# Performance work log

Hardware: AMD Instinct MI355X
Metric: run time of the kernel (lower is better)

The kernel has to match this reference:

```python
import jax, jax.numpy as jnp
import numpy as np

WS = 7          # window size
HN = 6          # heads
C = 192         # emb dim
SHIFT = WS >> 1
L = WS * WS


def _rel_index(ws):
    c = np.stack(np.meshgrid(np.arange(ws), np.arange(ws), indexing='ij'), -1).reshape(-1, 2)
    d = c[:, None, :] - c[None, :, :] + (ws - 1)
    return jnp.asarray(d[..., 0] * (2 * ws - 1) + d[..., 1])  # (L, L) int


def _shift_mask(ws, shift):
    # after intra-window roll by -shift, positions >= ws-shift are wrapped pixels
    r = (np.arange(ws) >= ws - shift).astype(np.int32)
    rid = (2 * r[:, None] + r[None, :]).reshape(-1)  # (L,) region id
    m = np.where(rid[:, None] != rid[None, :], -100.0, 0.0).astype(np.float32)
    return jnp.asarray(m)  # (L, L)


def _ln(x, g, b, eps=1e-5):
    m = jnp.mean(x, -1, keepdims=True)
    v = jnp.mean(jnp.square(x - m), -1, keepdims=True)
    return (x - m) * jax.lax.rsqrt(v + eps) * g + b


def _wmsa(x, qkv_w, qkv_b, proj_w, proj_b, bias_table, rel_idx, mask):
    N, wn, Lx, Cx = x.shape
    dh = Cx // HN
    qkv = x @ qkv_w + qkv_b                      # (N, wn, L, 3C)
    q, k, v = jnp.split(qkv, 3, axis=-1)
    q = q.reshape(N, wn, Lx, HN, dh) * (dh ** -0.5)
    k = k.reshape(N, wn, Lx, HN, dh)
    v = v.reshape(N, wn, Lx, HN, dh)
    a = jnp.einsum('nwqhd,nwkhd->nwhqk', q, k)   # (N, wn, H, L, L)
    a = a + jnp.transpose(bias_table[rel_idx], (2, 0, 1))  # (H, L, L) bias
    if mask is not None:
        a = a + mask                             # (L, L) broadcast
    a = jax.nn.softmax(a, axis=-1)
    o = jnp.einsum('nwhqk,nwkhd->nwqhd', a, v).reshape(N, wn, Lx, Cx)
    return o @ proj_w + proj_b


def _layer(X, g1, b1, g2, b2, qkv_w, qkv_b, proj_w, proj_b, bias_table, rel_idx,
           w1, bb1, w2, bb2, mask):
    tmp = _ln(X, g1, b1)
    tmp = _wmsa(tmp, qkv_w, qkv_b, proj_w, proj_b, bias_table, rel_idx, mask)
    X = _ln(X + tmp, g2, b2)  # drop_path is identity in eval
    h = jax.nn.gelu(X @ w1 + bb1, approximate=False)
    return X + (h @ w2 + bb2)


def setup_inputs() -> dict:
    key = jax.random.key(0)
    ks = jax.random.split(key, 16)
    N, wn = 8, 1024
    s = 0.02
    d = {}
    d['X'] = jax.random.normal(ks[0], (N, wn, L, C), jnp.float32)
    d['ln1_g'] = jnp.ones((C,), jnp.float32)
    d['ln1_b'] = jnp.zeros((C,), jnp.float32)
    d['ln2_g'] = jnp.ones((C,), jnp.float32)
    d['ln2_b'] = jnp.zeros((C,), jnp.float32)
    d['win_qkv_w'] = jax.random.normal(ks[1], (C, 3 * C), jnp.float32) * s
    d['win_qkv_b'] = jnp.zeros((3 * C,), jnp.float32)
    d['win_proj_w'] = jax.random.normal(ks[2], (C, C), jnp.float32) * s
    d['win_proj_b'] = jnp.zeros((C,), jnp.float32)
    d['win_bias'] = jax.random.normal(ks[3], ((2 * WS - 1) ** 2, HN), jnp.float32) * s
    d['swin_qkv_w'] = jax.random.normal(ks[4], (C, 3 * C), jnp.float32) * s
    d['swin_qkv_b'] = jnp.zeros((3 * C,), jnp.float32)
    d['swin_proj_w'] = jax.random.normal(ks[5], (C, C), jnp.float32) * s
    d['swin_proj_b'] = jnp.zeros((C,), jnp.float32)
    d['swin_bias'] = jax.random.normal(ks[6], ((2 * WS - 1) ** 2, HN), jnp.float32) * s
    d['mlp_w1'] = jax.random.normal(ks[7], (C, 4 * C), jnp.float32) * s
    d['mlp_b1'] = jnp.zeros((4 * C,), jnp.float32)
    d['mlp_w2'] = jax.random.normal(ks[8], (4 * C, C), jnp.float32) * s
    d['mlp_b2'] = jnp.zeros((C,), jnp.float32)
    return d


def reference(X, ln1_g, ln1_b, ln2_g, ln2_b,
              win_qkv_w, win_qkv_b, win_proj_w, win_proj_b, win_bias,
              swin_qkv_w, swin_qkv_b, swin_proj_w, swin_proj_b, swin_bias,
              mlp_w1, mlp_b1, mlp_w2, mlp_b2):
    rel_idx = _rel_index(WS)
    mask = _shift_mask(WS, SHIFT)
    N, wn = X.shape[0], X.shape[1]
    # block 1: plain window MSA
    X = _layer(X, ln1_g, ln1_b, ln2_g, ln2_b, win_qkv_w, win_qkv_b, win_proj_w,
               win_proj_b, win_bias, rel_idx, mlp_w1, mlp_b1, mlp_w2, mlp_b2, None)
    # intra-window cyclic shift (torch dims (-2,-3) = W,H axes)
    X = X.reshape(N, wn, WS, WS, C)
    X = jnp.roll(X, (-SHIFT, -SHIFT), axis=(3, 2))
    X = X.reshape(N, wn, L, C)
    # block 2: shifted window MSA with mask
    X = _layer(X, ln1_g, ln1_b, ln2_g, ln2_b, swin_qkv_w, swin_qkv_b, swin_proj_w,
               swin_proj_b, swin_bias, rel_idx, mlp_w1, mlp_b1, mlp_w2, mlp_b2, mask)
    # reverse roll — repo uses dims (-1,-2) = (C, W) axes; replicated faithfully
    X = X.reshape(N, wn, WS, WS, C)
    X = jnp.roll(X, (SHIFT, SHIFT), axis=(4, 3))
    return X.reshape(N, wn, L, C)
```

## Files before the change

### kernel.cpp

```cpp
#include <hip/hip_runtime.h>
#include <hip/hip_bf16.h>
#include <math.h>

#define NTOK 401408
#define NWIN 8192
#define NCHUNK 4
#define TOK_PER_CHUNK (NTOK / NCHUNK)
#define WIN_PER_CHUNK (NWIN / NCHUNK)

typedef __attribute__((ext_vector_type(8))) short bf16x8_t;
typedef __attribute__((ext_vector_type(4))) float f32x4_t;

__device__ __forceinline__ float bf2f(unsigned int u) {
    return __uint_as_float(u << 16);
}
__device__ __forceinline__ unsigned short f2bf(float f) {
    unsigned int x = __float_as_uint(f);
    x += 0x7fffu + ((x >> 16) & 1u);
    return (unsigned short)(x >> 16);
}
__device__ __forceinline__ unsigned int pack2bf(float a, float b) {
    return (unsigned int)f2bf(a) | ((unsigned int)f2bf(b) << 16);
}

__global__ void wt_all_kernel(const float* __restrict__ s0, const float* __restrict__ s1,
                              const float* __restrict__ s2, const float* __restrict__ s3,
                              const float* __restrict__ s4, const float* __restrict__ s5,
                              unsigned short* __restrict__ d0, unsigned short* __restrict__ d1,
                              unsigned short* __restrict__ d2, unsigned short* __restrict__ d3,
                              unsigned short* __restrict__ d4, unsigned short* __restrict__ d5) {
    int seg = blockIdx.y;
    const float* W; unsigned short* WT; int K, N;
    switch (seg) {
        case 0:  W = s0; WT = d0; K = 192; N = 576; break;
        case 1:  W = s1; WT = d1; K = 192; N = 576; break;
        case 2:  W = s2; WT = d2; K = 192; N = 192; break;
        case 3:  W = s3; WT = d3; K = 192; N = 192; break;
        case 4:  W = s4; WT = d4; K = 192; N = 768; break;
        default: W = s5; WT = d5; K = 768; N = 192; break;
    }
    int i = blockIdx.x * 256 + threadIdx.x;
    if (i >= N * K) return;
    int n = i / K, k = i - n * K;
    WT[i] = f2bf(W[(size_t)k * N + n]);
}

__global__ void bias_kernel(const float* __restrict__ bt0, const float* __restrict__ bt1,
                            float* __restrict__ bm) {
    int idx = blockIdx.x * 256 + threadIdx.x;
    int variant = blockIdx.y;
    const float* bt = variant ? bt1 : bt0;
    int r = idx & 3, lane = (idx >> 2) & 63, ni = (idx >> 8) & 3, mi = (idx >> 10) & 3, h = idx >> 12;
    int g = lane >> 4;
    int q = ni * 16 + (lane & 15);
    int k = mi * 16 + g * 4 + r;
    float v = 0.f;
    if (q < 49 && k < 49) {
        int qh = q / 7, qw = q - qh * 7, kh = k / 7, kw = k - kh * 7;
        v = bt[((qh - kh + 6) * 13 + (qw - kw + 6)) * 6 + h];
        if (variant) {
            int rq = 2 * (qh >= 4) + (qw >= 4), rk = 2 * (kh >= 4) + (kw >= 4);
            if (rq != rk) v -= 100.f;
        }
    }
    bm[(size_t)variant * 24576 + idx] = v;
}

template<int IN_BF16, int ROLL>
__global__ __launch_bounds__(256) void ln_kernel(const void* __restrict__ in,
                                                 unsigned short* __restrict__ out,
                                                 const float* __restrict__ g,
                                                 const float* __restrict__ b) {
    int tok  = blockIdx.x * 4 + (threadIdx.x >> 6);
    int lane = threadIdx.x & 63;
    int src = tok;
    if (ROLL) {
        int win = tok / 49, p2 = tok - win * 49;
        int h = p2 / 7, w = p2 - h * 7;
        int h2 = h + 3; if (h2 >= 7) h2 -= 7;
        int w2 = w + 3; if (w2 >= 7) w2 -= 7;
        src = win * 49 + h2 * 7 + w2;
    }
    float x0, x1, x2;
    if (IN_BF16) {
        const unsigned short* p = (const unsigned short*)in + (size_t)src * 192;
        x0 = bf2f(p[lane]); x1 = bf2f(p[lane + 64]); x2 = bf2f(p[lane + 128]);
    } else {
        const float* p = (const float*)in + (size_t)src * 192;
        x0 = p[lane]; x1 = p[lane + 64]; x2 = p[lane + 128];
    }
    float s  = x0 + x1 + x2;
    float sq = x0 * x0 + x1 * x1 + x2 * x2;
    for (int o = 32; o; o >>= 1) { s += __shfl_xor(s, o); sq += __shfl_xor(sq, o); }
    float m   = s * (1.f / 192.f);
    float var = sq * (1.f / 192.f) - m * m;
    float r   = rsqrtf(var + 1e-5f);
    unsigned short* q = out + (size_t)tok * 192;
    q[lane]       = f2bf((x0 - m) * r * g[lane]       + b[lane]);
    q[lane + 64]  = f2bf((x1 - m) * r * g[lane + 64]  + b[lane + 64]);
    q[lane + 128] = f2bf((x2 - m) * r * g[lane + 128] + b[lane + 128]);
}

#define EP_QKV        0
#define EP_PROJ1      1
#define EP_PROJ2      2
#define EP_MLP1       3
#define EP_MLP2_TRUNK 4
#define EP_MLP2_OUT   5

template<int NDIM, int KDIM, int NY, int EP>
__global__ __launch_bounds__(256) void gemm_kernel(const unsigned short* __restrict__ A,
                                                   const unsigned short* __restrict__ WT,
                                                   const float* __restrict__ bias,
                                                   const void* __restrict__ res,
                                                   void* __restrict__ out,
                                                   int row0) {
    __shared__ __align__(16) unsigned short As[128][40];
    __shared__ __align__(16) unsigned short Bs[96][40];
    int tid = threadIdx.x;
    int nwg = gridDim.x;
    int id = blockIdx.x;
    int id2 = (id & 7) * (nwg >> 3) + (id >> 3);
    int by = id2 % NY, bx = id2 / NY;
    int rowBase = bx * 128;
    int colBase = by * 96;

    int cr = tid >> 2, cp = (tid & 3) * 8;
    const unsigned short* Ab = A  + (size_t)rowBase * KDIM + cp;
    const unsigned short* Bb = WT + (size_t)colBase * KDIM + cp;

    uint4 a0, a1, b0, b1;
    const int NT = KDIM / 32;

    #define LOADK(k0)                                                          \
        do {                                                                   \
            a0 = *(const uint4*)(Ab + (size_t)cr * KDIM + (k0));               \
            a1 = *(const uint4*)(Ab + (size_t)(cr + 64) * KDIM + (k0));        \
            b0 = *(const uint4*)(Bb + (size_t)cr * KDIM + (k0));               \
            if (tid < 128) b1 = *(const uint4*)(Bb + (size_t)(cr + 64) * KDIM + (k0)); \
        } while (0)
    #define WRITEK()                                                           \
        do {                                                                   \
            *(uint4*)&As[cr][cp] = a0;                                         \
            *(uint4*)&As[cr + 64][cp] = a1;                                    \
            *(uint4*)&Bs[cr][cp] = b0;                                         \
            if (tid < 128) *(uint4*)&Bs[cr + 64][cp] = b1;                     \
        } while (0)

    LOADK(0);

    int wave = tid >> 6, lane = tid & 63;
    int wm = wave >> 1, wn = wave & 1;
    int kq = lane >> 4, lr = lane & 15;

    f32x4_t acc[4][3] = {};
    for (int kt = 0; kt < NT; ++kt) {
        __syncthreads();
        WRITEK();
        if (kt + 1 < NT) LOADK((kt + 1) * 32);
        __syncthreads();
        bf16x8_t afr[4], bfr[3];
        #pragma unroll
        for (int mi = 0; mi < 4; ++mi)
            afr[mi] = *(const bf16x8_t*)&As[wm * 64 + mi * 16 + lr][kq * 8];
        #pragma unroll
        for (int ni = 0; ni < 3; ++ni)
            bfr[ni] = *(const bf16x8_t*)&Bs[wn * 48 + ni * 16 + lr][kq * 8];
        #pragma unroll
        for (int mi = 0; mi < 4; ++mi)
            #pragma unroll
            for (int ni = 0; ni < 3; ++ni)
                acc[mi][ni] = __builtin_amdgcn_mfma_f32_16x16x32_bf16(
                    afr[mi], bfr[ni], acc[mi][ni], 0, 0, 0);
    }
    #undef LOADK
    #undef WRITEK

    const float* resf = (const float*)res;
    const unsigned short* resb = (const unsigned short*)res;
    #pragma unroll
    for (int mi = 0; mi < 4; ++mi) {
        #pragma unroll
        for (int ni = 0; ni < 3; ++ni) {
            int col = colBase + wn * 48 + ni * 16 + lr;
            float bcol = bias[col];
            #pragma unroll
            for (int r = 0; r < 4; ++r) {
                int rloc = rowBase + wm * 64 + mi * 16 + kq * 4 + r;
                float v = acc[mi][ni][r] + bcol;
                if (EP == EP_QKV) {
                    if (colBase < 192) v *= 0.17677669529663687f;
                    ((unsigned short*)out)[(size_t)rloc * NDIM + col] = f2bf(v);
                } else if (EP == EP_PROJ1) {
                    v += resf[(size_t)rloc * 192 + col];
                    ((unsigned short*)out)[(size_t)rloc * 192 + col] = f2bf(v);
                } else if (EP == EP_PROJ2) {
                    int win = rloc / 49, p2 = rloc - win * 49;
                    int h = p2 / 7, w = p2 - h * 7;
                    int h2 = h + 3; if (h2 >= 7) h2 -= 7;
                    int w2 = w + 3; if (w2 >= 7) w2 -= 7;
                    v += bf2f((unsigned int)resb[((size_t)win * 49 + h2 * 7 + w2) * 192 + col]);
                    ((unsigned short*)out)[(size_t)rloc * 192 + col] = f2bf(v);
                } else if (EP == EP_MLP1) {
                    float u2 = v * (1.59576912f + 0.0713548162f * v * v);
                    float e  = __expf(u2);
                    float gl = v - v * __builtin_amdgcn_rcpf(e + 1.f);
                    ((unsigned short*)out)[(size_t)rloc * NDIM + col] = f2bf(gl);
                } else if (EP == EP_MLP2_TRUNK) {
                    v += bf2f((unsigned int)resb[(size_t)rloc * 192 + col]);
                    int grow = row0 + rloc;
                    ((unsigned short*)out)[(size_t)grow * 192 + col] = f2bf(v);
                } else {
                    v += bf2f((unsigned int)resb[(size_t)rloc * 192 + col]);
                    int grow = row0 + rloc;
                    int win = grow / 49, p2 = grow - win * 49;
                    int h = p2 / 7, w = p2 - h * 7;
                    int w2 = w + 3; if (w2 >= 7) w2 -= 7;
                    int c2 = col + 3; if (c2 >= 192) c2 -= 192;
                    ((float*)out)[((size_t)win * 49 + h * 7 + w2) * 192 + c2] = v;
                }
            }
        }
    }
}

__global__ __launch_bounds__(64) void attn_kernel(const unsigned short* __restrict__ qkv,
                                                  const float* __restrict__ bm,
                                                  unsigned short* __restrict__ outp,
                                                  int win0) {
    __shared__ unsigned short P[64][72];
    __shared__ unsigned short VT[32][72];
    int head = blockIdx.x, wloc = blockIdx.y;
    int lane = threadIdx.x;
    int g = lane >> 4, lr = lane & 15;
    const unsigned short* base = qkv + (size_t)wloc * 49 * 576;

    for (int i = lane; i < 256; i += 64) {
        int tok = i >> 2, seg = i & 3;
        uint4 u = make_uint4(0u, 0u, 0u, 0u);
        if (tok < 49)
            u = *(const uint4*)(base + (size_t)tok * 576 + 384 + head * 32 + seg * 8);
        const unsigned short* us = (const unsigned short*)&u;
        #pragma unroll
        for (int j = 0; j < 8; ++j) VT[seg * 8 + j][tok] = us[j];
    }

    bf16x8_t kf[4], qf[4];
    #pragma unroll
    for (int mi = 0; mi < 4; ++mi) {
        int tok = mi * 16 + lr; if (tok > 48) tok = 48;
        kf[mi] = *(const bf16x8_t*)(base + (size_t)tok * 576 + 192 + head * 32 + g * 8);
    }
    #pragma unroll
    for (int ni = 0; ni < 4; ++ni) {
        int tok = ni * 16 + lr; if (tok > 48) tok = 48;
        qf[ni] = *(const bf16x8_t*)(base + (size_t)tok * 576 + head * 32 + g * 8);
    }

    const float* bmh = bm + (size_t)head * 4096;
    f32x4_t acc[4][4];
    #pragma unroll
    for (int mi = 0; mi < 4; ++mi)
        #pragma unroll
        for (int ni = 0; ni < 4; ++ni)
            acc[mi][ni] = *(const f32x4_t*)(bmh + ((mi * 4 + ni) * 64 + lane) * 4);
    #pragma unroll
    for (int mi = 0; mi < 4; ++mi)
        #pragma unroll
        for (int ni = 0; ni < 4; ++ni)
            acc[mi][ni] = __builtin_amdgcn_mfma_f32_16x16x32_bf16(kf[mi], qf[ni], acc[mi][ni], 0, 0, 0);

    float inv[4];
    #pragma unroll
    for (int ni = 0; ni < 4; ++ni) {
        float mx = -1e30f;
        #pragma unroll
        for (int mi = 0; mi < 3; ++mi)
            #pragma unroll
            for (int r = 0; r < 4; ++r) mx = fmaxf(mx, acc[mi][ni][r]);
        mx = fmaxf(mx, (g == 0) ? acc[3][ni][0] : -1e30f);
        mx = fmaxf(mx, __shfl_xor(mx, 16));
        mx = fmaxf(mx, __shfl_xor(mx, 32));
        float p[16], ss = 0.f;
        #pragma unroll
        for (int mi = 0; mi < 3; ++mi)
            #pragma unroll
            for (int r = 0; r < 4; ++r) {
                float e = __expf(acc[mi][ni][r] - mx);
                p[mi * 4 + r] = e; ss += e;
            }
        float e48 = (g == 0) ? __expf(acc[3][ni][0] - mx) : 0.f;
        p[12] = e48; p[13] = p[14] = p[15] = 0.f; ss += e48;
        ss += __shfl_xor(ss, 16);
        ss += __shfl_xor(ss, 32);
        inv[ni] = 1.f / ss;
        int q = ni * 16 + lr;
        #pragma unroll
        for (int mi = 0; mi < 4; ++mi) {
            *(unsigned int*)&P[q][mi * 16 + g * 4]     = pack2bf(p[mi * 4 + 0], p[mi * 4 + 1]);
            *(unsigned int*)&P[q][mi * 16 + g * 4 + 2] = pack2bf(p[mi * 4 + 2], p[mi * 4 + 3]);
        }
    }
    __syncthreads();

    f32x4_t oacc[2][4] = {};
    #pragma unroll
    for (int kt = 0; kt < 2; ++kt) {
        bf16x8_t va[2], pb[4];
        #pragma unroll
        for (int mt = 0; mt < 2; ++mt)
            va[mt] = *(const bf16x8_t*)&VT[mt * 16 + lr][kt * 32 + g * 8];
        #pragma unroll
        for (int nt = 0; nt < 4; ++nt)
            pb[nt] = *(const bf16x8_t*)&P[nt * 16 + lr][kt * 32 + g * 8];
        #pragma unroll
        for (int mt = 0; mt < 2; ++mt)
            #pragma unroll
            for (int nt = 0; nt < 4; ++nt)
                oacc[mt][nt] = __builtin_amdgcn_mfma_f32_16x16x32_bf16(va[mt], pb[nt], oacc[mt][nt], 0, 0, 0);
    }

    #pragma unroll
    for (int nt = 0; nt < 4; ++nt) {
        int q = nt * 16 + lr;
        if (q < 49) {
            size_t tokg = (size_t)(win0 + wloc) * 49 + q;
            unsigned short* op = outp + tokg * 192 + head * 32;
            #pragma unroll
            for (int mt = 0; mt < 2; ++mt) {
                int d0 = mt * 16 + g * 4;
                float a0 = oacc[mt][nt][0] * inv[nt], a1 = oacc[mt][nt][1] * inv[nt];
                float a2 = oacc[mt][nt][2] * inv[nt], a3 = oacc[mt][nt][3] * inv[nt];
                *(unsigned int*)(op + d0)     = pack2bf(a0, a1);
                *(unsigned int*)(op + d0 + 2) = pack2bf(a2, a3);
            }
        }
    }
}

extern "C" void kernel_launch(void* const* d_in, const int* in_sizes, int n_in,
                              void* d_out, int out_size, void* d_ws, size_t ws_size,
                              hipStream_t stream) {
    (void)in_sizes; (void)n_in; (void)out_size; (void)ws_size;
    const float* X     = (const float*)d_in[0];
    const float* ln1_g = (const float*)d_in[1];
    const float* ln1_b = (const float*)d_in[2];
    const float* ln2_g = (const float*)d_in[3];
    const float* ln2_b = (const float*)d_in[4];
    const float* qkv_w[2]  = { (const float*)d_in[5],  (const float*)d_in[10] };
    const float* qkv_b[2]  = { (const float*)d_in[6],  (const float*)d_in[11] };
    const float* proj_w[2] = { (const float*)d_in[7],  (const float*)d_in[12] };
    const float* proj_b[2] = { (const float*)d_in[8],  (const float*)d_in[13] };
    const float* btab[2]   = { (const float*)d_in[9],  (const float*)d_in[14] };
    const float* w1 = (const float*)d_in[15];
    const float* b1 = (const float*)d_in[16];
    const float* w2 = (const float*)d_in[17];
    const float* b2 = (const float*)d_in[18];

    char* p = (char*)d_ws;
    auto takeb = [&](size_t bytes) -> char* {
        char* r = p;
        p += (bytes + 255) & ~(size_t)255;
        return r;
    };
    auto take = [&](size_t elems) -> unsigned short* {
        return (unsigned short*)takeb(elems * 2);
    };
    unsigned short* WTq[2]; unsigned short* WTp[2];
    WTq[0] = take(576 * 192); WTp[0] = take(192 * 192);
    WTq[1] = take(576 * 192); WTp[1] = take(192 * 192);
    unsigned short* WT1 = take(768 * 192);
    unsigned short* WT2 = take(192 * 768);
    float* biasM = (float*)takeb(2 * 24576 * sizeof(float));
    unsigned short* B0 = take((size_t)NTOK * 192);
    unsigned short* B1 = take((size_t)TOK_PER_CHUNK * 768);
    unsigned short* TK = take((size_t)NTOK * 192);

    wt_all_kernel<<<dim3(576, 6), dim3(256), 0, stream>>>(
        qkv_w[0], qkv_w[1], proj_w[0], proj_w[1], w1, w2,
        WTq[0], WTq[1], WTp[0], WTp[1], WT1, WT2);
    bias_kernel<<<dim3(96, 2), dim3(256), 0, stream>>>(btab[0], btab[1], biasM);

    for (int blk = 0; blk < 2; ++blk) {
        if (blk == 0)
            ln_kernel<0, 0><<<dim3(NTOK / 4), dim3(256), 0, stream>>>((const void*)X, B0, ln1_g, ln1_b);
        else
            ln_kernel<1, 1><<<dim3(NTOK / 4), dim3(256), 0, stream>>>((const void*)TK, B0, ln1_g, ln1_b);

        for (int c = 0; c < NCHUNK; ++c) {
            int row0 = c * TOK_PER_CHUNK;
            gemm_kernel<576, 192, 6, EP_QKV><<<dim3((TOK_PER_CHUNK / 128) * 6), dim3(256), 0, stream>>>(
                B0 + (size_t)row0 * 192, WTq[blk], qkv_b[blk], nullptr, (void*)B1, row0);
            attn_kernel<<<dim3(6, WIN_PER_CHUNK), dim3(64), 0, stream>>>(
                B1, biasM + (size_t)blk * 24576, B0, c * WIN_PER_CHUNK);
        }

        if (blk == 0)
            gemm_kernel<192, 192, 2, EP_PROJ1><<<dim3((NTOK / 128) * 2), dim3(256), 0, stream>>>(
                B0, WTp[blk], proj_b[blk], (const void*)X, (void*)B1, 0);
        else
            gemm_kernel<192, 192, 2, EP_PROJ2><<<dim3((NTOK / 128) * 2), dim3(256), 0, stream>>>(
                B0, WTp[blk], proj_b[blk], (const void*)TK, (void*)B1, 0);

        ln_kernel<1, 0><<<dim3(NTOK / 4), dim3(256), 0, stream>>>((const void*)B1, B0, ln2_g, ln2_b);

        for (int c = 0; c < NCHUNK; ++c) {
            int row0 = c * TOK_PER_CHUNK;
            gemm_kernel<768, 192, 8, EP_MLP1><<<dim3((TOK_PER_CHUNK / 128) * 8), dim3(256), 0, stream>>>(
                B0 + (size_t)row0 * 192, WT1, b1, nullptr, (void*)B1, row0);
            if (blk == 0)
                gemm_kernel<192, 768, 2, EP_MLP2_TRUNK><<<dim3((TOK_PER_CHUNK / 128) * 2), dim3(256), 0, stream>>>(
                    B1, WT2, b2, (const void*)(B0 + (size_t)row0 * 192), (void*)TK, row0);
            else
                gemm_kernel<192, 768, 2, EP_MLP2_OUT><<<dim3((TOK_PER_CHUNK / 128) * 2), dim3(256), 0, stream>>>(
                    B1, WT2, b2, (const void*)(B0 + (size_t)row0 * 192), (void*)d_out, row0);
        }
    }
}
```

Measured before the change: 2.673 ms.

## Fuse projection GEMM with residual add and second LayerNorm

Replaces the projection GEMM epilogue plus the separate LayerNorm kernel with one kernel. Each workgroup computes all 192 output columns for 128 rows, adds bias and residual (rolled for block 2), and reduces mean and variance across lanes. It then writes the normalized bf16 result directly. This removes the intermediate B1 write and re-read and one kernel launch per block. In exchange it uses a wider tile with more accumulator registers, and it writes output in place over its own input buffer.

```diff
diff --git a/kernel.cpp b/kernel.cpp
--- a/kernel.cpp
+++ b/kernel.cpp
@@ -102,8 +102,6 @@
 }
 
 #define EP_QKV        0
-#define EP_PROJ1      1
-#define EP_PROJ2      2
 #define EP_MLP1       3
 #define EP_MLP2_TRUNK 4
 #define EP_MLP2_OUT   5
@@ -176,7 +174,6 @@
     #undef LOADK
     #undef WRITEK
 
-    const float* resf = (const float*)res;
     const unsigned short* resb = (const unsigned short*)res;
     #pragma unroll
     for (int mi = 0; mi < 4; ++mi) {
@@ -191,16 +188,6 @@
                 if (EP == EP_QKV) {
                     if (colBase < 192) v *= 0.17677669529663687f;
                     ((unsigned short*)out)[(size_t)rloc * NDIM + col] = f2bf(v);
-                } else if (EP == EP_PROJ1) {
-                    v += resf[(size_t)rloc * 192 + col];
-                    ((unsigned short*)out)[(size_t)rloc * 192 + col] = f2bf(v);
-                } else if (EP == EP_PROJ2) {
-                    int win = rloc / 49, p2 = rloc - win * 49;
-                    int h = p2 / 7, w = p2 - h * 7;
-                    int h2 = h + 3; if (h2 >= 7) h2 -= 7;
-                    int w2 = w + 3; if (w2 >= 7) w2 -= 7;
-                    v += bf2f((unsigned int)resb[((size_t)win * 49 + h2 * 7 + w2) * 192 + col]);
-                    ((unsigned short*)out)[(size_t)rloc * 192 + col] = f2bf(v);
                 } else if (EP == EP_MLP1) {
                     float u2 = v * (1.59576912f + 0.0713548162f * v * v);
                     float e  = __expf(u2);
@@ -224,6 +211,121 @@
     }
 }
 
+template<int ROLLRES>
+__global__ __launch_bounds__(256) void projln_kernel(const unsigned short* __restrict__ A,
+                                                     const unsigned short* __restrict__ WT,
+                                                     const float* __restrict__ bias,
+                                                     const void* __restrict__ res,
+                                                     const float* __restrict__ g2,
+                                                     const float* __restrict__ b2,
+                                                     unsigned short* __restrict__ out) {
+    __shared__ __align__(16) unsigned short As[128][40];
+    __shared__ __align__(16) unsigned short Bs[192][40];
+    int tid = threadIdx.x;
+    int nwg = gridDim.x;
+    int id = blockIdx.x;
+    int bx = (id & 7) * (nwg >> 3) + (id >> 3);
+    int rowBase = bx * 128;
+
+    int cr = tid >> 2, cp = (tid & 3) * 8;
+    const unsigned short* Ab = A  + (size_t)rowBase * 192 + cp;
+    const unsigned short* Bb = WT + cp;
+
+    uint4 a0, a1, b0, b1, b2r;
+    #define LOADK(k0)                                                          \
+        do {                                                                   \
+            a0  = *(const uint4*)(Ab + (size_t)cr * 192 + (k0));               \
+            a1  = *(const uint4*)(Ab + (size_t)(cr + 64) * 192 + (k0));        \
+            b0  = *(const uint4*)(Bb + (size_t)cr * 192 + (k0));               \
+            b1  = *(const uint4*)(Bb + (size_t)(cr + 64) * 192 + (k0));        \
+            b2r = *(const uint4*)(Bb + (size_t)(cr + 128) * 192 + (k0));       \
+        } while (0)
+    #define WRITEK()                                                           \
+        do {                                                                   \
+            *(uint4*)&As[cr][cp] = a0;                                         \
+            *(uint4*)&As[cr + 64][cp] = a1;                                    \
+            *(uint4*)&Bs[cr][cp] = b0;                                         \
+            *(uint4*)&Bs[cr + 64][cp] = b1;                                    \
+            *(uint4*)&Bs[cr + 128][cp] = b2r;                                  \
+        } while (0)
+
+    LOADK(0);
+
+    int wave = tid >> 6, lane = tid & 63;
+    int wm = wave;
+    int kq = lane >> 4, lr = lane & 15;
+
+    f32x4_t acc[2][12] = {};
+    for (int kt = 0; kt < 6; ++kt) {
+        __syncthreads();
+        WRITEK();
+        if (kt + 1 < 6) LOADK((kt + 1) * 32);
+        __syncthreads();
+        bf16x8_t afr[2], bfr[12];
+        #pragma unroll
+        for (int mi = 0; mi < 2; ++mi)
+            afr[mi] = *(const bf16x8_t*)&As[wm * 32 + mi * 16 + lr][kq * 8];
+        #pragma unroll
+        for (int ni = 0; ni < 12; ++ni)
+            bfr[ni] = *(const bf16x8_t*)&Bs[ni * 16 + lr][kq * 8];
+        #pragma unroll
+        for (int mi = 0; mi < 2; ++mi)
+            #pragma unroll
+            for (int ni = 0; ni < 12; ++ni)
+                acc[mi][ni] = __builtin_amdgcn_mfma_f32_16x16x32_bf16(
+                    afr[mi], bfr[ni], acc[mi][ni], 0, 0, 0);
+    }
+    #undef LOADK
+    #undef WRITEK
+
+    const float* resf = (const float*)res;
+    const unsigned short* resb = (const unsigned short*)res;
+    float biasv[12], g2v[12], b2v[12];
+    #pragma unroll
+    for (int ni = 0; ni < 12; ++ni) {
+        int col = ni * 16 + lr;
+        biasv[ni] = bias[col]; g2v[ni] = g2[col]; b2v[ni] = b2[col];
+    }
+
+    #pragma unroll
+    for (int mi = 0; mi < 2; ++mi) {
+        #pragma unroll
+        for (int r = 0; r < 4; ++r) {
+            int rloc = rowBase + wm * 32 + mi * 16 + kq * 4 + r;
+            size_t rsrc = rloc;
+            if (ROLLRES) {
+                int win = rloc / 49, p2 = rloc - win * 49;
+                int h = p2 / 7, w = p2 - h * 7;
+                int h2 = h + 3; if (h2 >= 7) h2 -= 7;
+                int w2 = w + 3; if (w2 >= 7) w2 -= 7;
+                rsrc = (size_t)win * 49 + h2 * 7 + w2;
+            }
+            float v[12], s = 0.f, sq = 0.f;
+            #pragma unroll
+            for (int ni = 0; ni < 12; ++ni) {
+                int col = ni * 16 + lr;
+                float t = acc[mi][ni][r] + biasv[ni];
+                t += ROLLRES ? bf2f((unsigned int)resb[rsrc * 192 + col])
+                             : resf[rsrc * 192 + col];
+                v[ni] = t; s += t; sq += t * t;
+            }
+            s  += __shfl_xor(s, 1);  s  += __shfl_xor(s, 2);
+            s  += __shfl_xor(s, 4);  s  += __shfl_xor(s, 8);
+            sq += __shfl_xor(sq, 1); sq += __shfl_xor(sq, 2);
+            sq += __shfl_xor(sq, 4); sq += __shfl_xor(sq, 8);
+            float mean = s * (1.f / 192.f);
+            float var  = sq * (1.f / 192.f) - mean * mean;
+            float rstd = rsqrtf(var + 1e-5f);
+            unsigned short* op = out + (size_t)rloc * 192;
+            #pragma unroll
+            for (int ni = 0; ni < 12; ++ni) {
+                int col = ni * 16 + lr;
+                op[col] = f2bf((v[ni] - mean) * rstd * g2v[ni] + b2v[ni]);
+            }
+        }
+    }
+}
+
 __global__ __launch_bounds__(64) void attn_kernel(const unsigned short* __restrict__ qkv,
                                                   const float* __restrict__ bm,
                                                   unsigned short* __restrict__ outp,
@@ -396,13 +498,11 @@
         }
 
         if (blk == 0)
-            gemm_kernel<192, 192, 2, EP_PROJ1><<<dim3((NTOK / 128) * 2), dim3(256), 0, stream>>>(
-                B0, WTp[blk], proj_b[blk], (const void*)X, (void*)B1, 0);
+            projln_kernel<0><<<dim3(NTOK / 128), dim3(256), 0, stream>>>(
+                B0, WTp[blk], proj_b[blk], (const void*)X, ln2_g, ln2_b, B0);
         else
-            gemm_kernel<192, 192, 2, EP_PROJ2><<<dim3((NTOK / 128) * 2), dim3(256), 0, stream>>>(
-                B0, WTp[blk], proj_b[blk], (const void*)TK, (void*)B1, 0);
-
-        ln_kernel<1, 0><<<dim3(NTOK / 4), dim3(256), 0, stream>>>((const void*)B1, B0, ln2_g, ln2_b);
+            projln_kernel<1><<<dim3(NTOK / 128), dim3(256), 0, stream>>>(
+                B0, WTp[blk], proj_b[blk], (const void*)TK, ln2_g, ln2_b, B0);
 
         for (int c = 0; c < NCHUNK; ++c) {
             int row0 = c * TOK_PER_CHUNK;
```

After: 2.536 ms. 1.05x faster.
